# Performance work log

Measured on AMD Instinct MI355X. Metric: run time of the kernel, lower is better.

## Reference

```python
import jax, jax.numpy as jnp
import numpy as np

B, S, D, H, E, K, DH = 4, 1024, 1024, 8, 4, 2, 128


def setup_inputs() -> dict:
    key = jax.random.key(0)
    ks = jax.random.split(key, 9)
    std = 1.0 / np.sqrt(D)
    f = lambda k, shape, s: jax.random.normal(k, shape, dtype=jnp.float32) * s
    return {
        'q_src': f(ks[0], (B, S, D), 1.0),
        'k_src': f(ks[1], (B, S, D), 1.0),
        'v_src': f(ks[2], (B, S, D), 1.0),
        'Wq': f(ks[3], (H * DH, D), std),
        'Wk': f(ks[4], (H * DH, D), std),
        'Wv': f(ks[5], (H * E, D, DH), std),
        'Wo': f(ks[6], (H * E, DH, D), 1.0 / np.sqrt(H * DH)),
        'sel_v': f(ks[7], (H * E, D), std),
        'sel_o': f(ks[8], (H * E, D), std),
    }


def _route(src, selw):
    # sigmoid-gated per-head top-k expert selection (get_sel), eval mode
    g = jax.nn.sigmoid((src @ selw.T).reshape(*src.shape[:-1], H, E))  # [B,S,H,E]
    val, idx = jax.lax.top_k(g, K)
    # dense per-expert mixture weights: zeros except top-k sigmoid gates
    return (jax.nn.one_hot(idx, E, dtype=g.dtype) * val[..., None]).sum(-2)  # [B,S,H,E]


def reference(q_src, k_src, v_src, Wq, Wk, Wv, Wo, sel_v, sel_o):
    scale = (1.0 / np.sqrt(DH)) ** 0.5  # scale.sqrt() applied to both q and k
    q = ((q_src @ Wq.T) * scale).reshape(B, S, H, DH).transpose(0, 2, 1, 3)  # [B,H,S,DH]
    k = ((k_src @ Wk.T) * scale).reshape(B, S, H, DH).transpose(0, 2, 1, 3)

    wv = _route(k_src, sel_v)  # [B,S,H,E] V-expert gates (from keys)
    wo = _route(q_src, sel_o)  # [B,S,H,E] O-expert gates (from queries)

    # cvmm V: per-token top-k mixture of expert V projections
    v_all = jnp.einsum('bsd,hedc->bshec', v_src, Wv.reshape(H, E, D, DH))
    v = jnp.einsum('bshec,bshe->bhsc', v_all, wv)  # [B,H,S,DH]

    att = jax.nn.softmax(jnp.einsum('bhqc,bhkc->bhqk', q, k), axis=-1)
    res = jnp.einsum('bhqk,bhkc->bqhc', att, v)  # [B,S,H,DH]

    # cvmm O: weight per-head outputs by gates, project and sum over heads/experts
    resw = res[..., None, :] * wo[..., None]  # [B,S,H,E,DH]
    out = jnp.einsum('bshec,hecd->bsd', resw, Wo.reshape(H, E, DH, D))
    return out
```

## Files before the change

### kernel.cpp

```cpp
#include <hip/hip_runtime.h>

#define DEV __device__ __forceinline__

typedef __attribute__((ext_vector_type(8))) short s8v;
typedef __attribute__((ext_vector_type(4))) short s4v;
typedef __attribute__((ext_vector_type(4))) float f4v;

DEV unsigned short f2b(float f){
    unsigned u = __float_as_uint(f);
    u = (u + 0x7FFFu + ((u >> 16) & 1u)) >> 16;
    return (unsigned short)u;
}
DEV float b2f(short s){ return __uint_as_float(((unsigned)(unsigned short)s) << 16); }

DEV void gload16(const void* g, void* l){
    __builtin_amdgcn_global_load_lds(
        (const __attribute__((address_space(1))) unsigned*)g,
        (__attribute__((address_space(3))) unsigned*)l, 16, 0, 0);
}


DEV void stage2(const short* A, const short* B, int sA, int sB, int kA, int kB,
                short* la, short* lb, int w, int lane){
    int srow = lane >> 3;
    int swcol = ((lane & 7) ^ srow) << 3;
    #pragma unroll
    for(int it = 0; it < 4; it++){
        int seg = (w << 2) + it;
        int row = (seg << 3) + srow;
        gload16(&A[(size_t)row * sA + kA + swcol], &la[seg << 9]);
        gload16(&B[(size_t)row * sB + kB + swcol], &lb[seg << 9]);
    }
}

DEV void mfma_block(const short* la, const short* lb, int wm, int wn, int qr, int grp, f4v acc[4][4]){
    #pragma unroll
    for(int ks = 0; ks < 2; ks++){
        s8v af[4], bf[4];
        #pragma unroll
        for(int m = 0; m < 4; m++)
            af[m] = *(const s8v*)&la[(wm + m * 16 + qr) * 64 + ((((ks << 2) + grp) ^ (qr & 7)) << 3)];
        #pragma unroll
        for(int n = 0; n < 4; n++)
            bf[n] = *(const s8v*)&lb[(wn + n * 16 + qr) * 64 + ((((ks << 2) + grp) ^ (qr & 7)) << 3)];
        #pragma unroll
        for(int m = 0; m < 4; m++)
            #pragma unroll
            for(int n = 0; n < 4; n++)
                acc[m][n] = __builtin_amdgcn_mfma_f32_16x16x32_bf16(af[m], bf[n], acc[m][n], 0, 0, 0);
    }
}

__global__ __launch_bounds__(256) void k_cvt(const float* s0, const float* s1, const float* s2,
                                             const float* s3, const float* s4,
                                             short* o0, short* o1, short* o2, short* o3, short* o4){
    int y = blockIdx.y;
    const float* s = (y == 0) ? s0 : (y == 1) ? s1 : (y == 2) ? s2 : (y == 3) ? s3 : s4;
    short* o = (y == 0) ? o0 : (y == 1) ? o1 : (y == 2) ? o2 : (y == 3) ? o3 : o4;
    int n8 = (y < 3) ? 524288 : 131072;
    int idx = blockIdx.x * 256 + threadIdx.x;
    if(idx < n8){
        const float4* f = (const float4*)(s + (size_t)idx * 8);
        float4 a = f[0], b = f[1];
        s8v v;
        v[0] = f2b(a.x); v[1] = f2b(a.y); v[2] = f2b(a.z); v[3] = f2b(a.w);
        v[4] = f2b(b.x); v[5] = f2b(b.y); v[6] = f2b(b.z); v[7] = f2b(b.w);
        *(s8v*)(o + (size_t)idx * 8) = v;
    }
}

__global__ __launch_bounds__(256) void k_transpose(const float* in, short* out, int R, int C){
    in  += (size_t)blockIdx.z * R * C;
    out += (size_t)blockIdx.z * R * C;
    __shared__ float t[32][33];
    int c0 = blockIdx.x * 32, r0 = blockIdx.y * 32;
    int tx = threadIdx.x & 31, ty = threadIdx.x >> 5;
    #pragma unroll
    for(int p = 0; p < 4; p++){
        int r = p * 8 + ty;
        t[r][tx] = in[(size_t)(r0 + r) * C + c0 + tx];
    }
    __syncthreads();
    #pragma unroll
    for(int p = 0; p < 4; p++){
        int c = p * 8 + ty;
        out[(size_t)(c0 + c) * R + r0 + tx] = (short)f2b(t[tx][c]);
    }
}

__global__ __launch_bounds__(256) void k_rlogits(const float* qsrc, const float* ksrc,
                                                 const float* selv, const float* selo,
                                                 float* part){
    int which = blockIdx.y;
    const float* src = which ? qsrc : ksrc;
    const float* sel = which ? selo : selv;
    int tt = blockIdx.x >> 3, ks = blockIdx.x & 7;
    int tok0 = tt << 7;
    __shared__ float lsrc[128][36];
    __shared__ float lsel[32][36];
    int tid = threadIdx.x;
    int ts = tid & 31, es = tid >> 5;
    float acc[4][4];
    #pragma unroll
    for(int j = 0; j < 4; j++)
        #pragma unroll
        for(int i = 0; i < 4; i++) acc[j][i] = 0.f;

    #pragma unroll 1
    for(int c = 0; c < 4; c++){
        int k0 = (ks << 7) + (c << 5);
        {
            int row = tid >> 1, half = tid & 1;
            const float4* g = (const float4*)(src + (size_t)(tok0 + row) * 1024 + k0 + half * 16);
            #pragma unroll
            for(int qq = 0; qq < 4; qq++){
                int qw = half * 4 + qq;
                *(float4*)&lsrc[row][((qw + row) & 7) * 4] = g[qq];
            }
        }
        {
            int row = tid >> 3, qw = tid & 7;
            *(float4*)&lsel[row][((qw + row) & 7) * 4] =
                *(const float4*)(sel + (size_t)row * 1024 + k0 + qw * 4);
        }
        __syncthreads();
        #pragma unroll
        for(int q = 0; q < 8; q++){
            float4 sv[4];
            #pragma unroll
            for(int i = 0; i < 4; i++){
                int e = es * 4 + i;
                sv[i] = *(const float4*)&lsel[e][((q + e) & 7) * 4];
            }
            int slot = ((q + ts) & 7) * 4;
            #pragma unroll
            for(int j = 0; j < 4; j++){
                float4 xv = *(const float4*)&lsrc[ts + 32 * j][slot];
                #pragma unroll
                for(int i = 0; i < 4; i++){
                    acc[j][i] = fmaf(xv.x, sv[i].x, acc[j][i]);
                    acc[j][i] = fmaf(xv.y, sv[i].y, acc[j][i]);
                    acc[j][i] = fmaf(xv.z, sv[i].z, acc[j][i]);
                    acc[j][i] = fmaf(xv.w, sv[i].w, acc[j][i]);
                }
            }
        }
        __syncthreads();
    }
    #pragma unroll
    for(int j = 0; j < 4; j++){
        int token = tok0 + ts + 32 * j;
        f4v st;
        #pragma unroll
        for(int i = 0; i < 4; i++) st[i] = acc[j][i];
        *(f4v*)&part[(((size_t)(ks * 2 + which) * 4096) + token) * 32 + es * 4] = st;
    }
}

__global__ __launch_bounds__(256) void k_rfinal(const float* part, float* wvp, float* wop){
    int which = blockIdx.y;
    float* wout = which ? wop : wvp;
    int tid = threadIdx.x;
    int tok = blockIdx.x * 32 + (tid >> 3), h = tid & 7;
    f4v sum = {0.f, 0.f, 0.f, 0.f};
    #pragma unroll
    for(int s = 0; s < 8; s++)
        sum += *(const f4v*)&part[(((size_t)(s * 2 + which) * 4096) + tok) * 32 + h * 4];
    float g[4];
    #pragma unroll
    for(int e = 0; e < 4; e++) g[e] = 1.0f / (1.0f + expf(-sum[e]));
    f4v out;
    #pragma unroll
    for(int e = 0; e < 4; e++){
        int rank = 0;
        #pragma unroll
        for(int j = 0; j < 4; j++)
            rank += (g[j] > g[e]) || (g[j] == g[e] && j < e);
        out[e] = (rank < 2) ? g[e] : 0.0f;
    }
    *(f4v*)&wout[(size_t)tok * 32 + h * 4] = out;
}

__global__ __launch_bounds__(256) void k_gemmqk(const short* qsb, const short* ksb,
                                                const short* wqb, const short* wkb,
                                                short* qo, short* ko, float scale){
    __shared__ __align__(16) short la[2][8192];
    __shared__ __align__(16) short lb[2][8192];
    int wg = (blockIdx.x & 7) * 64 + (blockIdx.x >> 3);
    int which = wg >> 8, tl = wg & 255;
    int mt = tl >> 3, nt = tl & 7;
    const short* A = (which ? ksb : qsb) + ((size_t)(mt << 7)) * 1024;
    const short* B = (which ? wkb : wqb) + ((size_t)(nt << 7)) * 1024;
    short* out = which ? ko : qo;
    int tid = threadIdx.x, lane = tid & 63, w = tid >> 6;
    int wm = (w >> 1) << 6, wn = (w & 1) << 6;
    int qr = lane & 15, grp = lane >> 4;
    f4v acc[4][4];
    #pragma unroll
    for(int m = 0; m < 4; m++)
        #pragma unroll
        for(int n = 0; n < 4; n++) acc[m][n] = f4v{0.f, 0.f, 0.f, 0.f};
    #pragma unroll 1
    for(int t = -1; t < 16; t++){
        int nxt = t + 1;
        if(nxt < 16)
            stage2(A, B, 1024, 1024, nxt << 6, nxt << 6, la[nxt & 1], lb[nxt & 1], w, lane);
        if(t >= 0)
            mfma_block(la[t & 1], lb[t & 1], wm, wn, qr, grp, acc);
        __syncthreads();
    }
    #pragma unroll
    for(int m = 0; m < 4; m++){
        int rb = (mt << 7) + wm + m * 16 + (grp << 2);
        #pragma unroll
        for(int n = 0; n < 4; n++){
            int col = (nt << 7) + wn + n * 16 + qr;
            #pragma unroll
            for(int r = 0; r < 4; r++)
                out[(size_t)(rb + r) * 1024 + col] = (short)f2b(acc[m][n][r] * scale);
        }
    }
}

__global__ __launch_bounds__(256) void k_gemmva(const short* A, const short* B, short* C){
    __shared__ __align__(16) short la[8192];
    __shared__ __align__(16) short lb[8192];
    int wg = (blockIdx.x & 7) * 128 + (blockIdx.x >> 3);
    int mt = wg >> 5, nt = wg & 31;
    int i0 = mt << 7, j0 = nt << 7;
    const short* Ab = A + (size_t)i0 * 1024;
    const short* Bb = B + (size_t)j0 * 1024;
    int tid = threadIdx.x, lane = tid & 63, w = tid >> 6;
    int wm = (w >> 1) << 6, wn = (w & 1) << 6;
    int qr = lane & 15, grp = lane >> 4;
    f4v acc[4][4];
    #pragma unroll
    for(int m = 0; m < 4; m++)
        #pragma unroll
        for(int n = 0; n < 4; n++) acc[m][n] = f4v{0.f, 0.f, 0.f, 0.f};
    #pragma unroll 1
    for(int t = 0; t < 16; t++){
        stage2(Ab, Bb, 1024, 1024, t << 6, t << 6, la, lb, w, lane);
        __syncthreads();
        mfma_block(la, lb, wm, wn, qr, grp, acc);
        __syncthreads();
    }
    #pragma unroll
    for(int m = 0; m < 4; m++){
        int rb = i0 + wm + m * 16 + (grp << 2);
        #pragma unroll
        for(int n = 0; n < 4; n++){
            int col = j0 + wn + n * 16 + qr;
            #pragma unroll
            for(int r = 0; r < 4; r++)
                C[(size_t)(rb + r) * 4096 + col] = (short)f2b(acc[m][n][r]);
        }
    }
}

__global__ __launch_bounds__(256) void k_vredg(const short* vall, const float* wv, short* vtg){
    int bh = blockIdx.y, b = bh >> 3, h = bh & 7;
    int s0 = blockIdx.x * 32;
    constexpr int LDT = 520;
    __shared__ __align__(16) short tile[32 * LDT];
    __shared__ float gsm[32][4];
    int tid = threadIdx.x;
    #pragma unroll
    for(int p = 0; p < 8; p++){
        int chunk = tid + p * 256;
        int row = chunk >> 6, cc = (chunk & 63) << 3;
        int token = b * 1024 + s0 + row;
        *(s8v*)&tile[row * LDT + cc] = *(const s8v*)&vall[(size_t)token * 4096 + h * 512 + cc];
    }
    if(tid < 128){
        int row = tid >> 2, e = tid & 3;
        gsm[row][e] = wv[(size_t)(b * 1024 + s0 + row) * 32 + h * 4 + e];
    }
    __syncthreads();
    #pragma unroll
    for(int p = 0; p < 16; p++){
        int idx = tid + p * 256;
        int s = idx & 31, c = idx >> 5;
        float v = 0.f;
        #pragma unroll
        for(int e = 0; e < 4; e++) v += b2f(tile[s * LDT + e * 128 + c]) * gsm[s][e];
        vtg[((size_t)bh * 128 + c) * 1024 + s0 + s] = (short)f2b(v);
    }
}

__global__ __launch_bounds__(256) void k_gemmo(const short* resw, const short* wot, float* po){
    __shared__ __align__(16) short la[2][8192];
    __shared__ __align__(16) short lb[2][8192];
    int wg = (blockIdx.x & 7) * 64 + (blockIdx.x >> 3);
    int ksp = wg & 1, tile = wg >> 1;
    int mt = tile >> 3, nt = tile & 7;
    const short* A = resw + (size_t)(mt << 7) * 4096 + ksp * 2048;
    const short* B = wot + (size_t)(nt << 7) * 4096 + ksp * 2048;
    int tid = threadIdx.x, lane = tid & 63, w = tid >> 6;
    int wm = (w >> 1) << 6, wn = (w & 1) << 6;
    int qr = lane & 15, grp = lane >> 4;
    f4v acc[4][4];
    #pragma unroll
    for(int m = 0; m < 4; m++)
        #pragma unroll
        for(int n = 0; n < 4; n++) acc[m][n] = f4v{0.f, 0.f, 0.f, 0.f};
    #pragma unroll 1
    for(int t = -1; t < 32; t++){
        int nxt = t + 1;
        if(nxt < 32)
            stage2(A, B, 4096, 4096, nxt << 6, nxt << 6, la[nxt & 1], lb[nxt & 1], w, lane);
        if(t >= 0)
            mfma_block(la[t & 1], lb[t & 1], wm, wn, qr, grp, acc);
        __syncthreads();
    }
    po += (size_t)ksp * 4194304;
    #pragma unroll
    for(int m = 0; m < 4; m++){
        int rb = (mt << 7) + wm + m * 16 + (grp << 2);
        #pragma unroll
        for(int n = 0; n < 4; n++){
            int col = (nt << 7) + wn + n * 16 + qr;
            #pragma unroll
            for(int r = 0; r < 4; r++)
                po[(size_t)(rb + r) * 1024 + col] = acc[m][n][r];
        }
    }
}

__global__ __launch_bounds__(256) void k_red(const float* p0, const float* p1, float* out){
    size_t idx = ((size_t)blockIdx.x * 256 + threadIdx.x) * 4;
    f4v a = *(const f4v*)&p0[idx];
    f4v b = *(const f4v*)&p1[idx];
    f4v s = a + b;
    *(f4v*)&out[idx] = s;
}

__global__ __launch_bounds__(256) void k_attn(const short* qg, const short* kg,
                                              const short* vtg, short* res){
    __shared__ __align__(16) short lk[2][8192];
    __shared__ __align__(16) short lv[2][8192];
    __shared__ __align__(16) short pl[4][16 * 72];
    int bh = blockIdx.y, b = bh >> 3, h = bh & 7;
    int w = threadIdx.x >> 6, lane = threadIdx.x & 63;
    int qr = lane & 15, grp = lane >> 4;
    int q0 = blockIdx.x * 64 + w * 16;
    const short* vtb = vtg + ((size_t)bh << 17);
    short* pw = &pl[w][0];

    int tok = b * 1024 + q0 + qr;
    s8v qf[4];
    #pragma unroll
    for(int ks = 0; ks < 4; ks++)
        qf[ks] = *(const s8v*)&qg[(size_t)tok * 1024 + h * 128 + ks * 32 + grp * 8];
    f4v o[8];
    #pragma unroll
    for(int ct = 0; ct < 8; ct++) o[ct] = f4v{0.f, 0.f, 0.f, 0.f};
    float m_cur = -1e30f, l_cur = 0.f;

    int klr = lane >> 4, klc = lane & 15;
    int vlr = lane >> 3, vlc = lane & 7;

    #pragma unroll 1
    for(int t = -1; t < 16; t++){
        int nxt = t + 1;
        if(nxt < 16){
            int buf = nxt & 1, kv0 = nxt << 6;
            #pragma unroll
            for(int i = 0; i < 4; i++){
                int seg = (w << 2) + i;
                int kr = (seg << 2) + klr;
                int kc = klc ^ (kr & 7);
                gload16(&kg[(size_t)(b * 1024 + kv0 + kr) * 1024 + h * 128 + kc * 8], &lk[buf][seg << 9]);
                int vr = (seg << 3) + vlr;
                int vc = vlc ^ (vr & 7);
                gload16(&vtb[(size_t)vr * 1024 + kv0 + vc * 8], &lv[buf][seg << 9]);
            }
        }
        if(t >= 0){
            int cur = t & 1;
            f4v s[4];
            #pragma unroll
            for(int kt = 0; kt < 4; kt++) s[kt] = f4v{0.f, 0.f, 0.f, 0.f};
            __builtin_amdgcn_s_setprio(1);
            #pragma unroll
            for(int ks = 0; ks < 4; ks++){
                #pragma unroll
                for(int kt = 0; kt < 4; kt++){
                    int row = kt * 16 + qr;
                    s8v kf = *(const s8v*)&lk[cur][row * 128 + ((((ks << 2) + grp) ^ (row & 7)) << 3)];
                    s[kt] = __builtin_amdgcn_mfma_f32_16x16x32_bf16(kf, qf[ks], s[kt], 0, 0, 0);
                }
            }
            __builtin_amdgcn_s_setprio(0);
            float pm = s[0][0];
            #pragma unroll
            for(int kt = 0; kt < 4; kt++)
                #pragma unroll
                for(int r = 0; r < 4; r++) pm = fmaxf(pm, s[kt][r]);
            pm = fmaxf(pm, __shfl_xor(pm, 16));
            pm = fmaxf(pm, __shfl_xor(pm, 32));
            float mn = fmaxf(m_cur, pm);
            float fs = __expf(m_cur - mn);
            float ps = 0.f;
            #pragma unroll
            for(int kt = 0; kt < 4; kt++)
                #pragma unroll
                for(int r = 0; r < 4; r++){
                    s[kt][r] = __expf(s[kt][r] - mn);
                    ps += s[kt][r];
                }
            ps += __shfl_xor(ps, 16);
            ps += __shfl_xor(ps, 32);
            l_cur = l_cur * fs + ps;
            m_cur = mn;
            #pragma unroll
            for(int ct = 0; ct < 8; ct++){
                o[ct][0] *= fs; o[ct][1] *= fs; o[ct][2] *= fs; o[ct][3] *= fs;
            }
            #pragma unroll
            for(int kt = 0; kt < 4; kt++){
                s4v pvv;
                #pragma unroll
                for(int r = 0; r < 4; r++) pvv[r] = (short)f2b(s[kt][r]);
                *(s4v*)&pw[qr * 72 + kt * 16 + grp * 4] = pvv;
            }
            s8v pf0 = *(const s8v*)&pw[qr * 72 + grp * 8];
            s8v pf1 = *(const s8v*)&pw[qr * 72 + 32 + grp * 8];
            __builtin_amdgcn_s_setprio(1);
            #pragma unroll
            for(int ct = 0; ct < 8; ct++){
                int row = ct * 16 + qr;
                s8v vf0 = *(const s8v*)&lv[cur][row * 64 + ((grp ^ (row & 7)) << 3)];
                s8v vf1 = *(const s8v*)&lv[cur][row * 64 + (((4 + grp) ^ (row & 7)) << 3)];
                o[ct] = __builtin_amdgcn_mfma_f32_16x16x32_bf16(vf0, pf0, o[ct], 0, 0, 0);
                o[ct] = __builtin_amdgcn_mfma_f32_16x16x32_bf16(vf1, pf1, o[ct], 0, 0, 0);
            }
            __builtin_amdgcn_s_setprio(0);
        }
        __syncthreads();
    }
    float inv = 1.0f / l_cur;
    #pragma unroll
    for(int ct = 0; ct < 8; ct++){
        s4v sv;
        #pragma unroll
        for(int r = 0; r < 4; r++) sv[r] = (short)f2b(o[ct][r] * inv);
        *(s4v*)&res[(size_t)tok * 1024 + h * 128 + ct * 16 + grp * 4] = sv;
    }
}

__global__ __launch_bounds__(256) void k_expand(const short* res, const float* wo, short* resw){
    int idx = blockIdx.x * 256 + threadIdx.x;
    int t = idx >> 9;
    int u = idx & 511;
    int he = u >> 4, ci = u & 15;
    int h = he >> 2;
    float g = wo[(size_t)t * 32 + he];
    s8v r = *(const s8v*)&res[(size_t)t * 1024 + h * 128 + ci * 8];
    s8v v;
    #pragma unroll
    for(int j = 0; j < 8; j++) v[j] = (short)f2b(b2f(r[j]) * g);
    *(s8v*)&resw[(size_t)t * 4096 + u * 8] = v;
}

extern "C" void kernel_launch(void* const* d_in, const int* in_sizes, int n_in,
                              void* d_out, int out_size, void* d_ws, size_t ws_size,
                              hipStream_t stream){
    const float* q_src = (const float*)d_in[0];
    const float* k_src = (const float*)d_in[1];
    const float* v_src = (const float*)d_in[2];
    const float* Wq    = (const float*)d_in[3];
    const float* Wk    = (const float*)d_in[4];
    const float* Wv    = (const float*)d_in[5];
    const float* Wo    = (const float*)d_in[6];
    const float* selv  = (const float*)d_in[7];
    const float* selo  = (const float*)d_in[8];

    const size_t MB = 1ull << 20;
    char* ws = (char*)d_ws;
    short* qsb  = (short*)(ws + 0 * MB);
    short* ksb  = (short*)(ws + 8 * MB);
    short* vsb  = (short*)(ws + 16 * MB);
    short* wqb  = (short*)(ws + 24 * MB);
    short* wkb  = (short*)(ws + 26 * MB);
    short* wvt  = (short*)(ws + 28 * MB);
    short* wot  = (short*)(ws + 36 * MB);
    short* q    = (short*)(ws + 44 * MB);
    short* k    = (short*)(ws + 52 * MB);
    short* vt   = (short*)(ws + 60 * MB);
    short* res  = (short*)(ws + 68 * MB);
    float* wv   = (float*)(ws + 76 * MB);
    float* wo   = (float*)(ws + 76 * MB + 524288);
    float* part = (float*)(ws + 80 * MB);
    short* vall = (short*)(ws + 80 * MB);
    float* po   = (float*)(ws + 80 * MB);
    short* resw = (short*)(ws + 0 * MB);

    const float qk_scale = 0.29730177875068026f;

    k_cvt<<<dim3(2048, 5), 256, 0, stream>>>(q_src, k_src, v_src, Wq, Wk, qsb, ksb, vsb, wqb, wkb);
    k_transpose<<<dim3(4, 32, 32), 256, 0, stream>>>(Wv, wvt, 1024, 128);
    k_transpose<<<dim3(32, 128, 1), 256, 0, stream>>>(Wo, wot, 4096, 1024);
    k_rlogits<<<dim3(256, 2), 256, 0, stream>>>(q_src, k_src, selv, selo, part);
    k_rfinal<<<dim3(128, 2), 256, 0, stream>>>(part, wv, wo);
    k_gemmqk<<<dim3(512), 256, 0, stream>>>(qsb, ksb, wqb, wkb, q, k, qk_scale);
    k_gemmva<<<dim3(1024), 256, 0, stream>>>(vsb, wvt, vall);
    k_vredg<<<dim3(32, 32), 256, 0, stream>>>(vall, wv, vt);
    k_attn<<<dim3(16, 32), 256, 0, stream>>>(q, k, vt, res);
    k_expand<<<dim3(8192), 256, 0, stream>>>(res, wo, resw);
    k_gemmo<<<dim3(512), 256, 0, stream>>>(resw, wot, po);
    k_red<<<dim3(4096), 256, 0, stream>>>(po, po + 4194304, (float*)d_out);
}
```

Baseline: 221.5 us.

## Replace V and O projection GEMMs with 256x256-tile 8-wave pipelined kernel

Adds a templated 512-thread GEMM with 256x256 output tiles, a 4-deep LDS ring fed by direct global-to-LDS loads, and interleaved MFMA and staging phases using barriers and s_setprio. It replaces both the V-expert projection GEMM and the output projection GEMM. The output GEMM moves from a 2-way to a 4-way K split, and the reduction kernel now sums four partial buffers, one pair of which reuses workspace freed after attention. Larger tiles are meant to raise data reuse and overlap loads with compute, at the cost of fewer workgroups (256), more LDS per block and more partial-sum traffic.

```diff
diff --git a/kernel.cpp b/kernel.cpp
--- a/kernel.cpp
+++ b/kernel.cpp
@@ -48,6 +48,127 @@
             #pragma unroll
             for(int n = 0; n < 4; n++)
                 acc[m][n] = __builtin_amdgcn_mfma_f32_16x16x32_bf16(af[m], bf[n], acc[m][n], 0, 0, 0);
+    }
+}
+
+template<int MODE>
+__global__ __launch_bounds__(512) void k_gemm8(const short* A, const short* B,
+                                               void* Cp, void* Cp2, int Ks, int NT){
+    __shared__ __align__(16) short la[4][8192];
+    __shared__ __align__(16) short lb[4][8192];
+    int nwg = gridDim.x;
+    int wg = ((int)blockIdx.x & 7) * (nwg >> 3) + ((int)blockIdx.x >> 3);
+    int mt, nt, kp = 0;
+    const short *Ab, *Bb;
+    if constexpr (MODE == 1){
+        kp = wg >> 6; mt = (wg >> 2) & 15; nt = wg & 3;
+        Ab = A + (size_t)(mt << 8) * Ks + (kp << 10);
+        Bb = B + (size_t)(nt << 8) * Ks + (kp << 10);
+    } else {
+        mt = wg >> 4; nt = wg & 15;
+        Ab = A + (size_t)(mt << 8) * Ks;
+        Bb = B + (size_t)(nt << 8) * Ks;
+    }
+    int tid = threadIdx.x, lane = tid & 63, w = tid >> 6;
+    int wr = w >> 2, wc = w & 3;
+    int qr = lane & 15, grp = lane >> 4;
+    int srow = lane >> 2, sc = lane & 3;
+    f4v acc[8][4];
+    #pragma unroll
+    for(int m = 0; m < 8; m++)
+        #pragma unroll
+        for(int n = 0; n < 4; n++) acc[m][n] = f4v{0.f, 0.f, 0.f, 0.f};
+
+    #define STAGE_A(t) { int tt = (t); \
+        _Pragma("unroll") \
+        for(int j = 0; j < 2; j++){ \
+            int seg = (j << 3) + w; \
+            int r = (seg << 4) + srow; \
+            int cg = sc ^ ((r >> 1) & 3); \
+            gload16(&Ab[(size_t)r * Ks + (tt << 5) + (cg << 3)], &la[tt & 3][seg << 9]); } }
+    #define STAGE_B(t) { int tt = (t); \
+        _Pragma("unroll") \
+        for(int j = 0; j < 2; j++){ \
+            int seg = (j << 3) + w; \
+            int r = (seg << 4) + srow; \
+            int cg = sc ^ ((r >> 1) & 3); \
+            gload16(&Bb[(size_t)r * Ks + (tt << 5) + (cg << 3)], &lb[tt & 3][seg << 9]); } }
+
+    STAGE_A(0); STAGE_B(0); STAGE_A(1); STAGE_B(1); STAGE_A(2); STAGE_B(2);
+    asm volatile("s_waitcnt vmcnt(8)" ::: "memory");
+    __builtin_amdgcn_s_barrier();
+
+    #pragma unroll 1
+    for(int t = 0; t < NT; t++){
+        const short* lat = &la[t & 3][0];
+        const short* lbt = &lb[t & 3][0];
+        s8v af[4], bf[4];
+        if(t + 3 < NT) STAGE_A(t + 3);
+        #pragma unroll
+        for(int n = 0; n < 4; n++){
+            int N = (wc << 6) + (n << 4) + qr;
+            bf[n] = *(const s8v*)&lbt[(N << 5) + ((grp ^ ((N >> 1) & 3)) << 3)];
+        }
+        #pragma unroll
+        for(int m = 0; m < 4; m++){
+            int M = (wr << 7) + (m << 4) + qr;
+            af[m] = *(const s8v*)&lat[(M << 5) + ((grp ^ ((M >> 1) & 3)) << 3)];
+        }
+        __builtin_amdgcn_s_barrier();
+        __builtin_amdgcn_s_setprio(1);
+        #pragma unroll
+        for(int m = 0; m < 4; m++)
+            #pragma unroll
+            for(int n = 0; n < 4; n++)
+                acc[m][n] = __builtin_amdgcn_mfma_f32_16x16x32_bf16(af[m], bf[n], acc[m][n], 0, 0, 0);
+        __builtin_amdgcn_s_setprio(0);
+        __builtin_amdgcn_s_barrier();
+        if(t + 3 < NT) STAGE_B(t + 3);
+        #pragma unroll
+        for(int m = 0; m < 4; m++){
+            int M = (wr << 7) + 64 + (m << 4) + qr;
+            af[m] = *(const s8v*)&lat[(M << 5) + ((grp ^ ((M >> 1) & 3)) << 3)];
+        }
+        __builtin_amdgcn_s_barrier();
+        __builtin_amdgcn_s_setprio(1);
+        #pragma unroll
+        for(int m = 0; m < 4; m++)
+            #pragma unroll
+            for(int n = 0; n < 4; n++)
+                acc[m + 4][n] = __builtin_amdgcn_mfma_f32_16x16x32_bf16(af[m], bf[n], acc[m + 4][n], 0, 0, 0);
+        __builtin_amdgcn_s_setprio(0);
+        asm volatile("s_waitcnt vmcnt(8)" ::: "memory");
+        __builtin_amdgcn_s_barrier();
+    }
+    #undef STAGE_A
+    #undef STAGE_B
+
+    if constexpr (MODE == 0){
+        short* C = (short*)Cp;
+        #pragma unroll
+        for(int m = 0; m < 8; m++){
+            int row = (mt << 8) + (wr << 7) + (m << 4) + (grp << 2);
+            #pragma unroll
+            for(int n = 0; n < 4; n++){
+                int col = (nt << 8) + (wc << 6) + (n << 4) + qr;
+                #pragma unroll
+                for(int r = 0; r < 4; r++)
+                    C[(size_t)(row + r) * 4096 + col] = (short)f2b(acc[m][n][r]);
+            }
+        }
+    } else {
+        float* C = (float*)((kp < 2) ? Cp : Cp2) + (size_t)(kp & 1) * 4194304;
+        #pragma unroll
+        for(int m = 0; m < 8; m++){
+            int row = (mt << 8) + (wr << 7) + (m << 4) + (grp << 2);
+            #pragma unroll
+            for(int n = 0; n < 4; n++){
+                int col = (nt << 8) + (wc << 6) + (n << 4) + qr;
+                #pragma unroll
+                for(int r = 0; r < 4; r++)
+                    C[(size_t)(row + r) * 1024 + col] = acc[m][n][r];
+            }
+        }
     }
 }
 
@@ -222,42 +343,6 @@
     }
 }
 
-__global__ __launch_bounds__(256) void k_gemmva(const short* A, const short* B, short* C){
-    __shared__ __align__(16) short la[8192];
-    __shared__ __align__(16) short lb[8192];
-    int wg = (blockIdx.x & 7) * 128 + (blockIdx.x >> 3);
-    int mt = wg >> 5, nt = wg & 31;
-    int i0 = mt << 7, j0 = nt << 7;
-    const short* Ab = A + (size_t)i0 * 1024;
-    const short* Bb = B + (size_t)j0 * 1024;
-    int tid = threadIdx.x, lane = tid & 63, w = tid >> 6;
-    int wm = (w >> 1) << 6, wn = (w & 1) << 6;
-    int qr = lane & 15, grp = lane >> 4;
-    f4v acc[4][4];
-    #pragma unroll
-    for(int m = 0; m < 4; m++)
-        #pragma unroll
-        for(int n = 0; n < 4; n++) acc[m][n] = f4v{0.f, 0.f, 0.f, 0.f};
-    #pragma unroll 1
-    for(int t = 0; t < 16; t++){
-        stage2(Ab, Bb, 1024, 1024, t << 6, t << 6, la, lb, w, lane);
-        __syncthreads();
-        mfma_block(la, lb, wm, wn, qr, grp, acc);
-        __syncthreads();
-    }
-    #pragma unroll
-    for(int m = 0; m < 4; m++){
-        int rb = i0 + wm + m * 16 + (grp << 2);
-        #pragma unroll
-        for(int n = 0; n < 4; n++){
-            int col = j0 + wn + n * 16 + qr;
-            #pragma unroll
-            for(int r = 0; r < 4; r++)
-                C[(size_t)(rb + r) * 4096 + col] = (short)f2b(acc[m][n][r]);
-        }
-    }
-}
-
 __global__ __launch_bounds__(256) void k_vredg(const short* vall, const float* wv, short* vtg){
     int bh = blockIdx.y, b = bh >> 3, h = bh & 7;
     int s0 = blockIdx.x * 32;
@@ -288,50 +373,11 @@
     }
 }
 
-__global__ __launch_bounds__(256) void k_gemmo(const short* resw, const short* wot, float* po){
-    __shared__ __align__(16) short la[2][8192];
-    __shared__ __align__(16) short lb[2][8192];
-    int wg = (blockIdx.x & 7) * 64 + (blockIdx.x >> 3);
-    int ksp = wg & 1, tile = wg >> 1;
-    int mt = tile >> 3, nt = tile & 7;
-    const short* A = resw + (size_t)(mt << 7) * 4096 + ksp * 2048;
-    const short* B = wot + (size_t)(nt << 7) * 4096 + ksp * 2048;
-    int tid = threadIdx.x, lane = tid & 63, w = tid >> 6;
-    int wm = (w >> 1) << 6, wn = (w & 1) << 6;
-    int qr = lane & 15, grp = lane >> 4;
-    f4v acc[4][4];
-    #pragma unroll
-    for(int m = 0; m < 4; m++)
-        #pragma unroll
-        for(int n = 0; n < 4; n++) acc[m][n] = f4v{0.f, 0.f, 0.f, 0.f};
-    #pragma unroll 1
-    for(int t = -1; t < 32; t++){
-        int nxt = t + 1;
-        if(nxt < 32)
-            stage2(A, B, 4096, 4096, nxt << 6, nxt << 6, la[nxt & 1], lb[nxt & 1], w, lane);
-        if(t >= 0)
-            mfma_block(la[t & 1], lb[t & 1], wm, wn, qr, grp, acc);
-        __syncthreads();
-    }
-    po += (size_t)ksp * 4194304;
-    #pragma unroll
-    for(int m = 0; m < 4; m++){
-        int rb = (mt << 7) + wm + m * 16 + (grp << 2);
-        #pragma unroll
-        for(int n = 0; n < 4; n++){
-            int col = (nt << 7) + wn + n * 16 + qr;
-            #pragma unroll
-            for(int r = 0; r < 4; r++)
-                po[(size_t)(rb + r) * 1024 + col] = acc[m][n][r];
-        }
-    }
-}
-
-__global__ __launch_bounds__(256) void k_red(const float* p0, const float* p1, float* out){
+__global__ __launch_bounds__(256) void k_red4(const float* p0, const float* p1,
+                                              const float* p2, const float* p3, float* out){
     size_t idx = ((size_t)blockIdx.x * 256 + threadIdx.x) * 4;
-    f4v a = *(const f4v*)&p0[idx];
-    f4v b = *(const f4v*)&p1[idx];
-    f4v s = a + b;
+    f4v s = (*(const f4v*)&p0[idx] + *(const f4v*)&p1[idx]) +
+            (*(const f4v*)&p2[idx] + *(const f4v*)&p3[idx]);
     *(f4v*)&out[idx] = s;
 }
 
@@ -493,8 +539,9 @@
     float* wo   = (float*)(ws + 76 * MB + 524288);
     float* part = (float*)(ws + 80 * MB);
     short* vall = (short*)(ws + 80 * MB);
-    float* po   = (float*)(ws + 80 * MB);
     short* resw = (short*)(ws + 0 * MB);
+    float* po01 = (float*)(ws + 44 * MB);
+    float* po23 = (float*)(ws + 80 * MB);
 
     const float qk_scale = 0.29730177875068026f;
 
@@ -504,10 +551,10 @@
     k_rlogits<<<dim3(256, 2), 256, 0, stream>>>(q_src, k_src, selv, selo, part);
     k_rfinal<<<dim3(128, 2), 256, 0, stream>>>(part, wv, wo);
     k_gemmqk<<<dim3(512), 256, 0, stream>>>(qsb, ksb, wqb, wkb, q, k, qk_scale);
-    k_gemmva<<<dim3(1024), 256, 0, stream>>>(vsb, wvt, vall);
+    k_gemm8<0><<<dim3(256), 512, 0, stream>>>(vsb, wvt, vall, nullptr, 1024, 32);
     k_vredg<<<dim3(32, 32), 256, 0, stream>>>(vall, wv, vt);
     k_attn<<<dim3(16, 32), 256, 0, stream>>>(q, k, vt, res);
     k_expand<<<dim3(8192), 256, 0, stream>>>(res, wo, resw);
-    k_gemmo<<<dim3(512), 256, 0, stream>>>(resw, wot, po);
-    k_red<<<dim3(4096), 256, 0, stream>>>(po, po + 4194304, (float*)d_out);
-}
+    k_gemm8<1><<<dim3(256), 512, 0, stream>>>(resw, wot, po01, po23, 4096, 32);
+    k_red4<<<dim3(4096), 256, 0, stream>>>(po01, po01 + 4194304, po23, po23 + 4194304, (float*)d_out);
+}
```

Result: slower. 242.5 us (+9.5%).

## Replace dense all-expert V projection with sparse gathered top-k expert GEMM

Applied to the files above, without the earlier changes.

Instead of computing the V projection for all 4 experts per head and then mixing them with gates, tokens routed to each (head, expert) pair are counted, scanned and gathered into padded 128-row groups. A grouped GEMM then computes only the selected expert projections with the gate applied. A combine kernel sums the two selected slots per token and writes the transposed V. This halves the V-projection FLOPs and the size of the intermediate, at the cost of three small routing kernels (one single-block scan, two 32-block passes), serial per-expert gather loops, and indirect row loads.

```diff
diff --git a/kernel.cpp b/kernel.cpp
--- a/kernel.cpp
+++ b/kernel.cpp
@@ -181,6 +181,174 @@
     *(f4v*)&wout[(size_t)tok * 32 + h * 4] = out;
 }
 
+__global__ __launch_bounds__(256) void k_count(const float* wv, int* cntv){
+    int he = blockIdx.x, tid = threadIdx.x;
+    __shared__ int red[256];
+    int c = 0;
+    #pragma unroll
+    for(int p = 0; p < 16; p++)
+        c += (wv[(size_t)(p * 256 + tid) * 32 + he] > 0.f) ? 1 : 0;
+    red[tid] = c;
+    __syncthreads();
+    for(int s = 128; s > 0; s >>= 1){
+        if(tid < s) red[tid] += red[tid + s];
+        __syncthreads();
+    }
+    if(tid == 0) cntv[he] = red[0];
+}
+
+__global__ __launch_bounds__(256) void k_scan(const int* cntv, int* basev, int* descv){
+    __shared__ int ntl[33];
+    int tid = threadIdx.x;
+    if(tid == 0){
+        int run = 0;
+        for(int he = 0; he < 32; he++){
+            ntl[he] = run;
+            run += (cntv[he] + 127) >> 7;
+        }
+        ntl[32] = run;
+    }
+    __syncthreads();
+    if(tid < 32) basev[tid] = ntl[tid] << 7;
+    for(int i = tid; i < 544; i += 256){
+        int d = -1;
+        for(int he = 0; he < 32; he++)
+            if(i >= ntl[he] && i < ntl[he + 1]) d = he;
+        descv[i] = d;
+    }
+}
+
+__global__ __launch_bounds__(256) void k_gather(const float* wv, const int* basev,
+                                                int* idxv, float* gbufv, int* rpos){
+    int he = blockIdx.x, h = he >> 2, e = he & 3;
+    int tid = threadIdx.x, lane = tid & 63, w = tid >> 6;
+    int base = basev[he];
+    __shared__ int wsum[4];
+    __shared__ int running;
+    if(tid == 0) running = 0;
+    __syncthreads();
+    #pragma unroll 1
+    for(int p = 0; p < 16; p++){
+        int t = p * 256 + tid;
+        float g = wv[(size_t)t * 32 + he];
+        bool sel = g > 0.f;
+        unsigned long long m = __ballot(sel);
+        int lpref = __popcll(m & ((1ull << lane) - 1ull));
+        if(lane == 0) wsum[w] = __popcll(m);
+        __syncthreads();
+        int rb = running;
+        int woff = 0;
+        #pragma unroll
+        for(int j = 0; j < 4; j++) woff += (j < w) ? wsum[j] : 0;
+        if(sel){
+            int pos = base + rb + woff + lpref;
+            idxv[pos] = t;
+            gbufv[pos] = g;
+            int slot = 0;
+            #pragma unroll
+            for(int j = 0; j < 4; j++)
+                slot += (j < e && wv[(size_t)t * 32 + h * 4 + j] > 0.f) ? 1 : 0;
+            rpos[(size_t)t * 16 + h * 2 + slot] = pos;
+        }
+        __syncthreads();
+        if(tid == 0) running += wsum[0] + wsum[1] + wsum[2] + wsum[3];
+        __syncthreads();
+    }
+    int tot = running;
+    int aligned = (tot + 127) & ~127;
+    for(int i = tid; i < aligned - tot; i += 256){
+        idxv[base + tot + i] = 0;
+        gbufv[base + tot + i] = 0.f;
+    }
+}
+
+__global__ __launch_bounds__(256) void k_gemmg(const short* vsb, const short* wvt,
+                                               const int* descv, const int* idxv,
+                                               const float* gbufv, short* Cg){
+    int he = descv[blockIdx.x];
+    if(he < 0) return;
+    int row0 = (int)blockIdx.x << 7;
+    __shared__ __align__(16) short la[2][8192];
+    __shared__ __align__(16) short lb[2][8192];
+    __shared__ int lidx[128];
+    int tid = threadIdx.x, lane = tid & 63, w = tid >> 6;
+    if(tid < 128) lidx[tid] = idxv[row0 + tid];
+    __syncthreads();
+    int srow = lane >> 3;
+    int swcol = ((lane & 7) ^ srow) << 3;
+    int arow[4];
+    #pragma unroll
+    for(int it = 0; it < 4; it++) arow[it] = lidx[(((w << 2) + it) << 3) + srow];
+    const short* Bb = wvt + ((size_t)he << 17);
+    int wm = (w >> 1) << 6, wn = (w & 1) << 6;
+    int qr = lane & 15, grp = lane >> 4;
+    f4v acc[4][4];
+    #pragma unroll
+    for(int m = 0; m < 4; m++)
+        #pragma unroll
+        for(int n = 0; n < 4; n++) acc[m][n] = f4v{0.f, 0.f, 0.f, 0.f};
+    #pragma unroll 1
+    for(int t = -1; t < 16; t++){
+        int nxt = t + 1;
+        if(nxt < 16){
+            int buf = nxt & 1, k0 = nxt << 6;
+            #pragma unroll
+            for(int it = 0; it < 4; it++){
+                int seg = (w << 2) + it;
+                int row = (seg << 3) + srow;
+                gload16(&vsb[(size_t)arow[it] * 1024 + k0 + swcol], &la[buf][seg << 9]);
+                gload16(&Bb[(size_t)row * 1024 + k0 + swcol], &lb[buf][seg << 9]);
+            }
+        }
+        if(t >= 0)
+            mfma_block(la[t & 1], lb[t & 1], wm, wn, qr, grp, acc);
+        __syncthreads();
+    }
+    #pragma unroll
+    for(int m = 0; m < 4; m++){
+        int rl = wm + m * 16 + (grp << 2);
+        #pragma unroll
+        for(int r = 0; r < 4; r++){
+            float g = gbufv[row0 + rl + r];
+            #pragma unroll
+            for(int n = 0; n < 4; n++){
+                int col = wn + n * 16 + qr;
+                Cg[(size_t)(row0 + rl + r) * 128 + col] = (short)f2b(acc[m][n][r] * g);
+            }
+        }
+    }
+}
+
+__global__ __launch_bounds__(256) void k_vcomb(const short* Cg, const int* rpos, short* vtg){
+    int bh = blockIdx.y, b = bh >> 3, h = bh & 7;
+    int s0 = blockIdx.x * 32;
+    __shared__ __align__(16) short t0[32][136];
+    __shared__ __align__(16) short t1[32][136];
+    __shared__ int rl[32][2];
+    int tid = threadIdx.x;
+    if(tid < 64){
+        int i = tid >> 1, s = tid & 1;
+        rl[i][s] = rpos[(size_t)(b * 1024 + s0 + i) * 16 + h * 2 + s];
+    }
+    __syncthreads();
+    #pragma unroll
+    for(int p = 0; p < 4; p++){
+        int ch = tid + p * 256;
+        int i = ch >> 5, slot = (ch >> 4) & 1, c8 = (ch & 15) << 3;
+        s8v v = *(const s8v*)&Cg[(size_t)rl[i][slot] * 128 + c8];
+        if(slot) *(s8v*)&t1[i][c8] = v;
+        else     *(s8v*)&t0[i][c8] = v;
+    }
+    __syncthreads();
+    #pragma unroll
+    for(int p = 0; p < 16; p++){
+        int idx = tid + p * 256;
+        int s = idx & 31, c = idx >> 5;
+        float v = b2f(t0[s][c]) + b2f(t1[s][c]);
+        vtg[((size_t)bh * 128 + c) * 1024 + s0 + s] = (short)f2b(v);
+    }
+}
+
 __global__ __launch_bounds__(256) void k_gemmqk(const short* qsb, const short* ksb,
                                                 const short* wqb, const short* wkb,
                                                 short* qo, short* ko, float scale){
@@ -219,72 +387,6 @@
             for(int r = 0; r < 4; r++)
                 out[(size_t)(rb + r) * 1024 + col] = (short)f2b(acc[m][n][r] * scale);
         }
-    }
-}
-
-__global__ __launch_bounds__(256) void k_gemmva(const short* A, const short* B, short* C){
-    __shared__ __align__(16) short la[8192];
-    __shared__ __align__(16) short lb[8192];
-    int wg = (blockIdx.x & 7) * 128 + (blockIdx.x >> 3);
-    int mt = wg >> 5, nt = wg & 31;
-    int i0 = mt << 7, j0 = nt << 7;
-    const short* Ab = A + (size_t)i0 * 1024;
-    const short* Bb = B + (size_t)j0 * 1024;
-    int tid = threadIdx.x, lane = tid & 63, w = tid >> 6;
-    int wm = (w >> 1) << 6, wn = (w & 1) << 6;
-    int qr = lane & 15, grp = lane >> 4;
-    f4v acc[4][4];
-    #pragma unroll
-    for(int m = 0; m < 4; m++)
-        #pragma unroll
-        for(int n = 0; n < 4; n++) acc[m][n] = f4v{0.f, 0.f, 0.f, 0.f};
-    #pragma unroll 1
-    for(int t = 0; t < 16; t++){
-        stage2(Ab, Bb, 1024, 1024, t << 6, t << 6, la, lb, w, lane);
-        __syncthreads();
-        mfma_block(la, lb, wm, wn, qr, grp, acc);
-        __syncthreads();
-    }
-    #pragma unroll
-    for(int m = 0; m < 4; m++){
-        int rb = i0 + wm + m * 16 + (grp << 2);
-        #pragma unroll
-        for(int n = 0; n < 4; n++){
-            int col = j0 + wn + n * 16 + qr;
-            #pragma unroll
-            for(int r = 0; r < 4; r++)
-                C[(size_t)(rb + r) * 4096 + col] = (short)f2b(acc[m][n][r]);
-        }
-    }
-}
-
-__global__ __launch_bounds__(256) void k_vredg(const short* vall, const float* wv, short* vtg){
-    int bh = blockIdx.y, b = bh >> 3, h = bh & 7;
-    int s0 = blockIdx.x * 32;
-    constexpr int LDT = 520;
-    __shared__ __align__(16) short tile[32 * LDT];
-    __shared__ float gsm[32][4];
-    int tid = threadIdx.x;
-    #pragma unroll
-    for(int p = 0; p < 8; p++){
-        int chunk = tid + p * 256;
-        int row = chunk >> 6, cc = (chunk & 63) << 3;
-        int token = b * 1024 + s0 + row;
-        *(s8v*)&tile[row * LDT + cc] = *(const s8v*)&vall[(size_t)token * 4096 + h * 512 + cc];
-    }
-    if(tid < 128){
-        int row = tid >> 2, e = tid & 3;
-        gsm[row][e] = wv[(size_t)(b * 1024 + s0 + row) * 32 + h * 4 + e];
-    }
-    __syncthreads();
-    #pragma unroll
-    for(int p = 0; p < 16; p++){
-        int idx = tid + p * 256;
-        int s = idx & 31, c = idx >> 5;
-        float v = 0.f;
-        #pragma unroll
-        for(int e = 0; e < 4; e++) v += b2f(tile[s * LDT + e * 128 + c]) * gsm[s][e];
-        vtg[((size_t)bh * 128 + c) * 1024 + s0 + s] = (short)f2b(v);
     }
 }
 
@@ -492,9 +594,15 @@
     float* wv   = (float*)(ws + 76 * MB);
     float* wo   = (float*)(ws + 76 * MB + 524288);
     float* part = (float*)(ws + 80 * MB);
-    short* vall = (short*)(ws + 80 * MB);
+    short* Cg   = (short*)(ws + 80 * MB);
+    int*   cntv = (int*)  (ws + 100 * MB);
+    int*   basev= (int*)  (ws + 100 * MB + 4096);
+    int*   descv= (int*)  (ws + 100 * MB + 8192);
+    int*   idxv = (int*)  (ws + 101 * MB);
+    float* gbufv= (float*)(ws + 102 * MB);
+    int*   rposv= (int*)  (ws + 103 * MB);
+    short* resw = (short*)(ws + 0 * MB);
     float* po   = (float*)(ws + 80 * MB);
-    short* resw = (short*)(ws + 0 * MB);
 
     const float qk_scale = 0.29730177875068026f;
 
@@ -503,9 +611,12 @@
     k_transpose<<<dim3(32, 128, 1), 256, 0, stream>>>(Wo, wot, 4096, 1024);
     k_rlogits<<<dim3(256, 2), 256, 0, stream>>>(q_src, k_src, selv, selo, part);
     k_rfinal<<<dim3(128, 2), 256, 0, stream>>>(part, wv, wo);
+    k_count<<<dim3(32), 256, 0, stream>>>(wv, cntv);
+    k_scan<<<dim3(1), 256, 0, stream>>>(cntv, basev, descv);
+    k_gather<<<dim3(32), 256, 0, stream>>>(wv, basev, idxv, gbufv, rposv);
     k_gemmqk<<<dim3(512), 256, 0, stream>>>(qsb, ksb, wqb, wkb, q, k, qk_scale);
-    k_gemmva<<<dim3(1024), 256, 0, stream>>>(vsb, wvt, vall);
-    k_vredg<<<dim3(32, 32), 256, 0, stream>>>(vall, wv, vt);
+    k_gemmg<<<dim3(544), 256, 0, stream>>>(vsb, wvt, descv, idxv, gbufv, Cg);
+    k_vcomb<<<dim3(32, 32), 256, 0, stream>>>(Cg, rposv, vt);
     k_attn<<<dim3(16, 32), 256, 0, stream>>>(q, k, vt, res);
     k_expand<<<dim3(8192), 256, 0, stream>>>(res, wo, resw);
     k_gemmo<<<dim3(512), 256, 0, stream>>>(resw, wot, po);
```

New measurement: 230.0 us. 3.9% more time.
